# Optimization experiments

Hardware: AMD Instinct MI355X
Metric: run time of the kernel (lower is better)

The kernel has to match this reference:

```python
import jax, jax.numpy as jnp
import numpy as np

NUM_ORI = 20
DEGREE = 2
EPS = 1e-5

def _gelu(x):
    return jax.nn.gelu(x, approximate=False)

def _poly(x, degree=DEGREE):
    # PolynomialFeatures: concat of tensor powers 1..degree+1 of last dim
    feats = [x]
    cur = x
    for _ in range(degree):
        cur = (cur[..., :, None] * x[..., None, :]).reshape(x.shape[:-1] + (-1,))
        feats.append(cur)
    return jnp.concatenate(feats, axis=-1)

def setup_inputs():
    key = jax.random.key(0)
    ks = jax.random.split(key, 16)
    B, N, O, Cin, C, L = 1, 160, NUM_ORI, 16, 128, 2
    basis = C
    def w(k, shape, fan_in):
        return jax.random.normal(k, shape, jnp.float32) / np.sqrt(fan_in).astype(np.float32)
    return {
        "x": jax.random.normal(ks[0], (B, N, O, Cin), jnp.float32),
        "pos": jax.random.normal(ks[1], (B, N, 2), jnp.float32),
        "bw1": w(ks[2], (14, C), 14), "bb1": jnp.zeros((C,), jnp.float32),
        "bw2": w(ks[3], (C, basis), C), "bb2": jnp.zeros((basis,), jnp.float32),
        "fw1": w(ks[4], (3, C), 3), "fb1": jnp.zeros((C,), jnp.float32),
        "fw2": w(ks[5], (C, basis), C), "fb2": jnp.zeros((basis,), jnp.float32),
        "emb_w": w(ks[6], (Cin, C), Cin),
        "kernel_w": w(ks[7], (L, basis, C), basis),
        "fiber_w": w(ks[8], (L, basis, C), basis),
        "conv_b": jnp.zeros((L, C), jnp.float32),
        "ln_g": jnp.ones((L, C), jnp.float32), "ln_b": jnp.zeros((L, C), jnp.float32),
        "mlp_w1": w(ks[9], (L, C, 4 * C), C), "mlp_b1": jnp.zeros((L, 4 * C), jnp.float32),
        "mlp_w2": w(ks[10], (L, 4 * C, C), 4 * C), "mlp_b2": jnp.zeros((L, C), jnp.float32),
    }

def reference(x, pos, bw1, bb1, bw2, bb2, fw1, fb1, fw2, fb2, emb_w,
              kernel_w, fiber_w, conv_b, ln_g, ln_b, mlp_w1, mlp_b1, mlp_w2, mlp_b2):
    # uniform grid of orientations on the circle (GridGenerator(2, num_ori))
    theta = jnp.arange(NUM_ORI, dtype=jnp.float32) * (2.0 * jnp.pi / NUM_ORI)
    ori = jnp.stack([jnp.cos(theta), jnp.sin(theta)], axis=-1)              # [O,2]
    rel = pos[:, None, :, None, :] - pos[:, :, None, None, :]               # [B,M,N,1,2]
    inv1 = jnp.sum(rel * ori[None, None, None], axis=-1, keepdims=True)     # [B,M,N,O,1]
    inv2 = jnp.linalg.norm(rel - rel * inv1, axis=-1, keepdims=True)        # [B,M,N,O,1]
    spat = jnp.concatenate([inv1, inv2], axis=-1)                           # [B,M,N,O,2]
    kb = _gelu(_gelu(_poly(spat) @ bw1 + bb1) @ bw2 + bb2)                  # [B,M,N,O,basis]
    oi = jnp.sum(ori[:, None] * ori[None], axis=-1, keepdims=True)          # [P,O,1]
    fkb = _gelu(_gelu(_poly(oi) @ fw1 + fb1) @ fw2 + fb2)                   # [P,O,basis]
    h = x @ emb_w                                                           # [B,N,O,C]
    C = emb_w.shape[1]
    for l in range(kernel_w.shape[0]):
        kern = kb @ kernel_w[l]                                             # [B,M,N,O,C]
        fk = fkb @ fiber_w[l]                                               # [P,O,C]
        x1 = jnp.einsum('bnoc,bmnoc->bmoc', h, kern)                        # spatial conv
        x2 = jnp.einsum('bmoc,poc->bmpc', x1, fk) / C + conv_b[l]           # fiber conv (depthwise)
        mu = jnp.mean(x2, axis=-1, keepdims=True)
        var = jnp.var(x2, axis=-1, keepdims=True)
        xn = (x2 - mu) / jnp.sqrt(var + EPS) * ln_g[l] + ln_b[l]            # LayerNorm
        mid = _gelu(xn @ mlp_w1[l] + mlp_b1[l])                             # bottleneck MLP
        h = h + (mid @ mlp_w2[l] + mlp_b2[l])                               # residual (layer_scale=None)
    return h
```

## Files before the change

### kernel.cpp

```cpp
#include <hip/hip_runtime.h>
#include <math.h>

#define NORI 20
#define NPTS 160
#define CDIM 128
#define TWO_PI_OVER_O (6.28318530717958647692f / 20.0f)
#define SW 132
#define SAS 136
#define SCL 256.0f
#define ISCL 0.00390625f

typedef __attribute__((ext_vector_type(8))) _Float16 half8v;
typedef __attribute__((ext_vector_type(4))) float float4v;

__device__ __forceinline__ float gelu_exact(float x) {
    float t  = 0.70710678118654752440f * x;
    float at = fabsf(t);
    float tau = __builtin_amdgcn_rcpf(fmaf(0.3275911f, at, 1.0f));
    float p = fmaf(1.061405429f, tau, -1.453152027f);
    p = fmaf(p, tau, 1.421413741f);
    p = fmaf(p, tau, -0.284496736f);
    p = fmaf(p, tau, 0.254829592f);
    p = p * tau;
    float e = __expf(-t * t);
    float erf_abs = fmaf(-p, e, 1.0f);
    float erf_t = copysignf(erf_abs, t);
    return 0.5f * x * (1.0f + erf_t);
}
__device__ __forceinline__ float4 ld4(const float* p) { return *(const float4*)p; }
__device__ __forceinline__ unsigned short f16b(float f) {
    _Float16 h = (_Float16)f;
    return __builtin_bit_cast(unsigned short, h);
}
__device__ __forceinline__ float f16tof(unsigned short u) {
    return (float)__builtin_bit_cast(_Float16, u);
}

#define FMA4(d, s, v) { d.x += (s)*(v).x; d.y += (s)*(v).y; d.z += (s)*(v).z; d.w += (s)*(v).w; }
#define GELU4(d) { d.x = gelu_exact(d.x); d.y = gelu_exact(d.y); \
                   d.z = gelu_exact(d.z); d.w = gelu_exact(d.w); }

__global__ __launch_bounds__(128) void fk_kernel(
    const float* __restrict__ fw1, const float* __restrict__ fb1,
    const float* __restrict__ fw2, const float* __restrict__ fb2,
    const float* __restrict__ fiber_w, unsigned short* __restrict__ fk)
{
    __shared__ float s_u[CDIM];
    __shared__ float s_z[CDIM];
    int bid = blockIdx.x;
    int l = bid / 400;
    int rem = bid % 400;
    int p = rem / 20, o = rem % 20;
    int j = threadIdx.x;

    float t = cosf(TWO_PI_OVER_O * (float)(p - o));
    float f1 = t * t, f2 = f1 * t;

    float u = gelu_exact(t * fw1[j] + f1 * fw1[CDIM + j] + f2 * fw1[2 * CDIM + j] + fb1[j]);
    s_u[j] = u;
    __syncthreads();

    float z0 = 0.f, z1 = 0.f, z2 = 0.f, z3 = 0.f;
    for (int i = 0; i < CDIM; i += 4) {
        z0 += s_u[i    ] * fw2[(i    ) * CDIM + j];
        z1 += s_u[i + 1] * fw2[(i + 1) * CDIM + j];
        z2 += s_u[i + 2] * fw2[(i + 2) * CDIM + j];
        z3 += s_u[i + 3] * fw2[(i + 3) * CDIM + j];
    }
    float z = gelu_exact(((z0 + z1) + (z2 + z3)) + fb2[j]);
    s_z[j] = z;
    __syncthreads();

    const float* fw = fiber_w + l * CDIM * CDIM;
    float a0 = 0.f, a1 = 0.f, a2 = 0.f, a3 = 0.f;
    for (int i = 0; i < CDIM; i += 4) {
        a0 += s_z[i    ] * fw[(i    ) * CDIM + j];
        a1 += s_z[i + 1] * fw[(i + 1) * CDIM + j];
        a2 += s_z[i + 2] * fw[(i + 2) * CDIM + j];
        a3 += s_z[i + 3] * fw[(i + 3) * CDIM + j];
    }
    fk[bid * CDIM + j] = f16b((a0 + a1) + (a2 + a3));
}

__global__ __launch_bounds__(128) void h0_kernel(
    const float* __restrict__ x, const float* __restrict__ emb_w,
    float* __restrict__ h)
{
    int row = blockIdx.x;
    int j = threadIdx.x;
    const float* xr = x + row * 16;
    float acc = 0.f;
#pragma unroll
    for (int i = 0; i < 16; ++i) acc += xr[i] * emb_w[i * CDIM + j];
    h[row * CDIM + j] = acc;
}

__global__ __launch_bounds__(128) void wt_kernel(
    const float* __restrict__ bw2, const float* __restrict__ kernel_w,
    unsigned short* __restrict__ wt)
{
    int b = blockIdx.x;
    int mat = b >> 7, c = b & 127;
    const float* src = (mat == 0) ? bw2 : (kernel_w + (mat - 1) * CDIM * CDIM);
    int k = threadIdx.x;
    wt[(mat * CDIM + c) * CDIM + k] = f16b(src[k * CDIM + c]);
}

#define FOR_BANDS(X) X(0) X(1) X(2) X(3) X(4) X(5) X(6) X(7) X(8) X(9)

#define DECL_ACC(B) float4v acc##B##_0 = {0.f,0.f,0.f,0.f}, acc##B##_1 = {0.f,0.f,0.f,0.f};

#define LDB(PTR, COL, KT) (*(const half8v*)((PTR) + (COL) * CDIM + (KT) * 32 + lh8))

#define LOADB(P, PTR) \
    half8v P##0_0 = LDB(PTR, col0, 0), P##0_1 = LDB(PTR, col1, 0); \
    half8v P##1_0 = LDB(PTR, col0, 1), P##1_1 = LDB(PTR, col1, 1); \
    half8v P##2_0 = LDB(PTR, col0, 2), P##2_1 = LDB(PTR, col1, 2); \
    half8v P##3_0 = LDB(PTR, col0, 3), P##3_1 = LDB(PTR, col1, 3);

#define G_BAND(B, P) { \
    const unsigned short* ar_ = s_act + (B) * 16 * SAS + abase; \
    half8v a0_ = *(const half8v*)(ar_); \
    half8v a1_ = *(const half8v*)(ar_ + 32); \
    half8v a2_ = *(const half8v*)(ar_ + 64); \
    half8v a3_ = *(const half8v*)(ar_ + 96); \
    acc##B##_0 = __builtin_amdgcn_mfma_f32_16x16x32_f16(a0_, P##0_0, acc##B##_0, 0, 0, 0); \
    acc##B##_1 = __builtin_amdgcn_mfma_f32_16x16x32_f16(a0_, P##0_1, acc##B##_1, 0, 0, 0); \
    acc##B##_0 = __builtin_amdgcn_mfma_f32_16x16x32_f16(a1_, P##1_0, acc##B##_0, 0, 0, 0); \
    acc##B##_1 = __builtin_amdgcn_mfma_f32_16x16x32_f16(a1_, P##1_1, acc##B##_1, 0, 0, 0); \
    acc##B##_0 = __builtin_amdgcn_mfma_f32_16x16x32_f16(a2_, P##2_0, acc##B##_0, 0, 0, 0); \
    acc##B##_1 = __builtin_amdgcn_mfma_f32_16x16x32_f16(a2_, P##2_1, acc##B##_1, 0, 0, 0); \
    acc##B##_0 = __builtin_amdgcn_mfma_f32_16x16x32_f16(a3_, P##3_0, acc##B##_0, 0, 0, 0); \
    acc##B##_1 = __builtin_amdgcn_mfma_f32_16x16x32_f16(a3_, P##3_1, acc##B##_1, 0, 0, 0); }

#define G1(B) G_BAND(B, bwf)
#define G2(B) G_BAND(B, kwf)

#define ZW_BAND(B) { \
    int rb_ = (B) * 16 + lh4; \
    s_act[(rb_ + 0) * SAS + col0] = f16b(gelu_exact(fmaf(SCL, acc##B##_0.x, zb0)) * ISCL); \
    s_act[(rb_ + 1) * SAS + col0] = f16b(gelu_exact(fmaf(SCL, acc##B##_0.y, zb0)) * ISCL); \
    s_act[(rb_ + 2) * SAS + col0] = f16b(gelu_exact(fmaf(SCL, acc##B##_0.z, zb0)) * ISCL); \
    s_act[(rb_ + 3) * SAS + col0] = f16b(gelu_exact(fmaf(SCL, acc##B##_0.w, zb0)) * ISCL); \
    s_act[(rb_ + 0) * SAS + col1] = f16b(gelu_exact(fmaf(SCL, acc##B##_1.x, zb1)) * ISCL); \
    s_act[(rb_ + 1) * SAS + col1] = f16b(gelu_exact(fmaf(SCL, acc##B##_1.y, zb1)) * ISCL); \
    s_act[(rb_ + 2) * SAS + col1] = f16b(gelu_exact(fmaf(SCL, acc##B##_1.z, zb1)) * ISCL); \
    s_act[(rb_ + 3) * SAS + col1] = f16b(gelu_exact(fmaf(SCL, acc##B##_1.w, zb1)) * ISCL); \
    acc##B##_0 = vzero; acc##B##_1 = vzero; }

#define H_BAND(B) { \
    int nb_ = (B) * 16 + lh4; \
    xacc0 += acc##B##_0.x * hb0[(nb_ + 0) * 2560]; \
    xacc0 += acc##B##_0.y * hb0[(nb_ + 1) * 2560]; \
    xacc0 += acc##B##_0.z * hb0[(nb_ + 2) * 2560]; \
    xacc0 += acc##B##_0.w * hb0[(nb_ + 3) * 2560]; \
    xacc1 += acc##B##_1.x * hb1[(nb_ + 0) * 2560]; \
    xacc1 += acc##B##_1.y * hb1[(nb_ + 1) * 2560]; \
    xacc1 += acc##B##_1.z * hb1[(nb_ + 2) * 2560]; \
    xacc1 += acc##B##_1.w * hb1[(nb_ + 3) * 2560]; }

__global__ __launch_bounds__(256, 2) void x1_kernel(
    const float* __restrict__ pos, const float* __restrict__ h,
    const float* __restrict__ bw1, const float* __restrict__ bb1,
    const float* __restrict__ bb2,
    const unsigned short* __restrict__ wtb,
    const unsigned short* __restrict__ wtk,
    float* __restrict__ x1)
{
    __shared__ __align__(16) unsigned short s_act[160 * SAS];
    __shared__ float s_bw1[9 * SW];
    __shared__ float s_bb1[CDIM];

    const int tid = threadIdx.x;
    const int rg = tid & 15;
    const int cgv = tid >> 4;
    const int c0u = cgv << 3;

    if (tid < CDIM) {
        const int c = tid;
        s_bw1[0 * SW + c] = bw1[0 * CDIM + c];
        s_bw1[1 * SW + c] = bw1[1 * CDIM + c];
        s_bw1[2 * SW + c] = bw1[2 * CDIM + c];
        s_bw1[3 * SW + c] = bw1[3 * CDIM + c] + bw1[4 * CDIM + c];
        s_bw1[4 * SW + c] = bw1[5 * CDIM + c];
        s_bw1[5 * SW + c] = bw1[6 * CDIM + c];
        s_bw1[6 * SW + c] = bw1[7 * CDIM + c] + bw1[8 * CDIM + c] + bw1[10 * CDIM + c];
        s_bw1[7 * SW + c] = bw1[9 * CDIM + c] + bw1[11 * CDIM + c] + bw1[12 * CDIM + c];
        s_bw1[8 * SW + c] = bw1[13 * CDIM + c];
        s_bb1[c] = bb1[c];
    }

    const int m = blockIdx.x / NORI;
    const int o = blockIdx.x % NORI;
    const float th = TWO_PI_OVER_O * (float)o;
    const float ox = cosf(th), oy = sinf(th);
    const float pmx = pos[2 * m], pmy = pos[2 * m + 1];

    __syncthreads();

#pragma unroll
    for (int rr = 0; rr < 10; ++rr) {
        const int row = rr * 16 + rg;
        float rx = pos[2 * row] - pmx, ry = pos[2 * row + 1] - pmy;
        float ia = rx * ox + ry * oy;
        float ib = sqrtf(rx * rx + ry * ry) * fabsf(1.0f - ia);
        float q2a = ia * ia, q2m = ia * ib, q2b = ib * ib;
        float q3a = q2a * ia, q3m = q2a * ib, q3n = q2m * ib, q3b = q2b * ib;
        float4 ua = ld4(&s_bb1[c0u]);
        float4 ub = ld4(&s_bb1[c0u + 4]);
#define UF(I, S) { float4 wa_ = ld4(&s_bw1[(I) * SW + c0u]); \
                   float4 wb_ = ld4(&s_bw1[(I) * SW + c0u + 4]); \
                   FMA4(ua, S, wa_); FMA4(ub, S, wb_); }
        UF(0, ia) UF(1, ib) UF(2, q2a) UF(3, q2m) UF(4, q2b)
        UF(5, q3a) UF(6, q3m) UF(7, q3n) UF(8, q3b)
#undef UF
        GELU4(ua) GELU4(ub)
        uint4 up;
        up.x = (unsigned int)f16b(ua.x * ISCL) | ((unsigned int)f16b(ua.y * ISCL) << 16);
        up.y = (unsigned int)f16b(ua.z * ISCL) | ((unsigned int)f16b(ua.w * ISCL) << 16);
        up.z = (unsigned int)f16b(ub.x * ISCL) | ((unsigned int)f16b(ub.y * ISCL) << 16);
        up.w = (unsigned int)f16b(ub.z * ISCL) | ((unsigned int)f16b(ub.w * ISCL) << 16);
        *(uint4*)&s_act[row * SAS + c0u] = up;
    }

    const int lane = tid & 63;
    const int wv = tid >> 6;
    const int li = lane & 15;
    const int lh = lane >> 4;
    const int lh8 = lh << 3, lh4 = lh << 2;
    const int col0 = wv * 32 + li;
    const int col1 = col0 + 16;
    const int abase = li * SAS + lh8;
    const float4v vzero = {0.f, 0.f, 0.f, 0.f};

    FOR_BANDS(DECL_ACC)
    LOADB(bwf, wtb)
    __syncthreads();

    FOR_BANDS(G1)
    __syncthreads();

    const float zb0 = bb2[col0], zb1 = bb2[col1];
    FOR_BANDS(ZW_BAND)
    LOADB(kwf, wtk)
    __syncthreads();

    FOR_BANDS(G2)

    const float* hb0 = h + o * CDIM + col0;
    const float* hb1 = h + o * CDIM + col1;
    float xacc0 = 0.f, xacc1 = 0.f;
    FOR_BANDS(H_BAND)

    xacc0 += __shfl_xor(xacc0, 16, 64);
    xacc0 += __shfl_xor(xacc0, 32, 64);
    xacc1 += __shfl_xor(xacc1, 16, 64);
    xacc1 += __shfl_xor(xacc1, 32, 64);

    if (lane < 16) {
        float* x1p = x1 + (m * NORI + o) * CDIM;
        x1p[col0] = xacc0 * SCL;
        x1p[col1] = xacc1 * SCL;
    }
}

__global__ __launch_bounds__(128) void mlp_kernel(
    const float* __restrict__ x1, const unsigned short* __restrict__ fk_l,
    const float* __restrict__ conv_b, const float* __restrict__ ln_g,
    const float* __restrict__ ln_b,
    const float* __restrict__ w1, const float* __restrict__ b1,
    const float* __restrict__ w2, const float* __restrict__ b2,
    float* __restrict__ h)
{
    __shared__ float s_xn[4][132];
    __shared__ float s_mid[4][520];
    __shared__ float s_s1[4][2], s_sq[4][2];

    const int c = threadIdx.x;
    const int m = blockIdx.x / 5, pg = blockIdx.x % 5;
    const int lane = c & 63, wid = c >> 6;

    float x1v[NORI];
#pragma unroll
    for (int o = 0; o < NORI; ++o) x1v[o] = x1[(m * NORI + o) * CDIM + c];

    float x2v[4];
#pragma unroll
    for (int rr = 0; rr < 4; ++rr) {
        int p = pg * 4 + rr;
        float x2 = 0.f;
#pragma unroll
        for (int o = 0; o < NORI; ++o) x2 += x1v[o] * f16tof(fk_l[(p * NORI + o) * CDIM + c]);
        x2 = x2 * (1.0f / 128.0f) + conv_b[c];
        x2v[rr] = x2;
        float s1 = x2, sq = x2 * x2;
        for (int off = 32; off; off >>= 1) {
            s1 += __shfl_down(s1, off, 64);
            sq += __shfl_down(sq, off, 64);
        }
        if (lane == 0) { s_s1[rr][wid] = s1; s_sq[rr][wid] = sq; }
    }
    __syncthreads();
#pragma unroll
    for (int rr = 0; rr < 4; ++rr) {
        float mu  = (s_s1[rr][0] + s_s1[rr][1]) * (1.0f / 128.0f);
        float var = (s_sq[rr][0] + s_sq[rr][1]) * (1.0f / 128.0f) - mu * mu;
        float xn = (x2v[rr] - mu) * rsqrtf(var + 1e-5f) * ln_g[c] + ln_b[c];
        s_xn[rr][c] = xn;
    }
    __syncthreads();

#pragma unroll
    for (int kq = 0; kq < 4; ++kq) {
        int k = kq * CDIM + c;
        float b = b1[k];
        float ac0 = b, ac1 = b, ac2 = b, ac3 = b;
        for (int i = 0; i < CDIM; ++i) {
            float w = w1[i * 512 + k];
            ac0 += s_xn[0][i] * w;
            ac1 += s_xn[1][i] * w;
            ac2 += s_xn[2][i] * w;
            ac3 += s_xn[3][i] * w;
        }
        s_mid[0][k] = gelu_exact(ac0);
        s_mid[1][k] = gelu_exact(ac1);
        s_mid[2][k] = gelu_exact(ac2);
        s_mid[3][k] = gelu_exact(ac3);
    }
    __syncthreads();

    float ao0 = 0.f, ao1 = 0.f, ao2 = 0.f, ao3 = 0.f;
    for (int k = 0; k < 512; ++k) {
        float w = w2[k * CDIM + c];
        ao0 += s_mid[0][k] * w;
        ao1 += s_mid[1][k] * w;
        ao2 += s_mid[2][k] * w;
        ao3 += s_mid[3][k] * w;
    }
    float bb = b2[c];
    h[(m * NORI + pg * 4 + 0) * CDIM + c] += ao0 + bb;
    h[(m * NORI + pg * 4 + 1) * CDIM + c] += ao1 + bb;
    h[(m * NORI + pg * 4 + 2) * CDIM + c] += ao2 + bb;
    h[(m * NORI + pg * 4 + 3) * CDIM + c] += ao3 + bb;
}

extern "C" void kernel_launch(void* const* d_in, const int* in_sizes, int n_in,
                              void* d_out, int out_size, void* d_ws, size_t ws_size,
                              hipStream_t stream)
{
    const float* x        = (const float*)d_in[0];
    const float* pos      = (const float*)d_in[1];
    const float* bw1      = (const float*)d_in[2];
    const float* bb1      = (const float*)d_in[3];
    const float* bw2      = (const float*)d_in[4];
    const float* bb2      = (const float*)d_in[5];
    const float* fw1      = (const float*)d_in[6];
    const float* fb1      = (const float*)d_in[7];
    const float* fw2      = (const float*)d_in[8];
    const float* fb2      = (const float*)d_in[9];
    const float* emb_w    = (const float*)d_in[10];
    const float* kernel_w = (const float*)d_in[11];
    const float* fiber_w  = (const float*)d_in[12];
    const float* conv_b   = (const float*)d_in[13];
    const float* ln_g     = (const float*)d_in[14];
    const float* ln_b     = (const float*)d_in[15];
    const float* mlp_w1   = (const float*)d_in[16];
    const float* mlp_b1   = (const float*)d_in[17];
    const float* mlp_w2   = (const float*)d_in[18];
    const float* mlp_b2   = (const float*)d_in[19];

    float* h = (float*)d_out;

    unsigned short* wt = (unsigned short*)d_ws;
    unsigned short* fk = wt + 3 * CDIM * CDIM;
    float* x1 = (float*)(fk + 2 * NORI * NORI * CDIM);

    wt_kernel<<<3 * CDIM, 128, 0, stream>>>(bw2, kernel_w, wt);
    fk_kernel<<<2 * NORI * NORI, 128, 0, stream>>>(fw1, fb1, fw2, fb2, fiber_w, fk);
    h0_kernel<<<NPTS * NORI, 128, 0, stream>>>(x, emb_w, h);

    for (int l = 0; l < 2; ++l) {
        x1_kernel<<<NPTS * NORI, 256, 0, stream>>>(
            pos, h, bw1, bb1, bb2, wt, wt + (1 + l) * CDIM * CDIM, x1);
        mlp_kernel<<<NPTS * NORI / 4, 128, 0, stream>>>(
            x1, fk + l * NORI * NORI * CDIM,
            conv_b + l * CDIM, ln_g + l * CDIM, ln_b + l * CDIM,
            mlp_w1 + l * CDIM * 4 * CDIM, mlp_b1 + l * 4 * CDIM,
            mlp_w2 + l * 4 * CDIM * CDIM, mlp_b2 + l * CDIM, h);
    }
}
```

Baseline: 318.1 us.

## Split x1 kernel across eight waves with one MFMA column tile each

The x1 kernel moves from 256 to 512 threads per block. Each wave now owns a single 16-column output tile instead of two, which halves the accumulator registers per lane and the per-thread work in the basis-feature stage. The launch bound is raised to allow more resident waves to hide latency. Smaller tweaks rewrite GELU as a single fma on |x/2| and pack f16 pairs with cvt_pkrtz, which changes rounding to round-toward-zero. The trade-off is more threads contending for the same LDS and syncthreads per block.

```diff
diff --git a/kernel.cpp b/kernel.cpp
--- a/kernel.cpp
+++ b/kernel.cpp
@@ -24,8 +24,8 @@
     p = p * tau;
     float e = __expf(-t * t);
     float erf_abs = fmaf(-p, e, 1.0f);
-    float erf_t = copysignf(erf_abs, t);
-    return 0.5f * x * (1.0f + erf_t);
+    float hx = 0.5f * x;
+    return fmaf(fabsf(hx), erf_abs, hx);
 }
 __device__ __forceinline__ float4 ld4(const float* p) { return *(const float4*)p; }
 __device__ __forceinline__ unsigned short f16b(float f) {
@@ -34,6 +34,10 @@
 }
 __device__ __forceinline__ float f16tof(unsigned short u) {
     return (float)__builtin_bit_cast(_Float16, u);
+}
+__device__ __forceinline__ unsigned int pkrtz(float a, float b) {
+    auto h = __builtin_amdgcn_cvt_pkrtz(a, b);
+    return __builtin_bit_cast(unsigned int, h);
 }
 
 #define FMA4(d, s, v) { d.x += (s)*(v).x; d.y += (s)*(v).y; d.z += (s)*(v).z; d.w += (s)*(v).w; }
@@ -108,15 +112,15 @@
 
 #define FOR_BANDS(X) X(0) X(1) X(2) X(3) X(4) X(5) X(6) X(7) X(8) X(9)
 
-#define DECL_ACC(B) float4v acc##B##_0 = {0.f,0.f,0.f,0.f}, acc##B##_1 = {0.f,0.f,0.f,0.f};
-
-#define LDB(PTR, COL, KT) (*(const half8v*)((PTR) + (COL) * CDIM + (KT) * 32 + lh8))
+#define DECL_ACC(B) float4v acc##B = {0.f,0.f,0.f,0.f};
+
+#define LDB(PTR, KT) (*(const half8v*)((PTR) + col0 * CDIM + (KT) * 32 + lh8))
 
 #define LOADB(P, PTR) \
-    half8v P##0_0 = LDB(PTR, col0, 0), P##0_1 = LDB(PTR, col1, 0); \
-    half8v P##1_0 = LDB(PTR, col0, 1), P##1_1 = LDB(PTR, col1, 1); \
-    half8v P##2_0 = LDB(PTR, col0, 2), P##2_1 = LDB(PTR, col1, 2); \
-    half8v P##3_0 = LDB(PTR, col0, 3), P##3_1 = LDB(PTR, col1, 3);
+    half8v P##0 = LDB(PTR, 0); \
+    half8v P##1 = LDB(PTR, 1); \
+    half8v P##2 = LDB(PTR, 2); \
+    half8v P##3 = LDB(PTR, 3);
 
 #define G_BAND(B, P) { \
     const unsigned short* ar_ = s_act + (B) * 16 * SAS + abase; \
@@ -124,42 +128,30 @@
     half8v a1_ = *(const half8v*)(ar_ + 32); \
     half8v a2_ = *(const half8v*)(ar_ + 64); \
     half8v a3_ = *(const half8v*)(ar_ + 96); \
-    acc##B##_0 = __builtin_amdgcn_mfma_f32_16x16x32_f16(a0_, P##0_0, acc##B##_0, 0, 0, 0); \
-    acc##B##_1 = __builtin_amdgcn_mfma_f32_16x16x32_f16(a0_, P##0_1, acc##B##_1, 0, 0, 0); \
-    acc##B##_0 = __builtin_amdgcn_mfma_f32_16x16x32_f16(a1_, P##1_0, acc##B##_0, 0, 0, 0); \
-    acc##B##_1 = __builtin_amdgcn_mfma_f32_16x16x32_f16(a1_, P##1_1, acc##B##_1, 0, 0, 0); \
-    acc##B##_0 = __builtin_amdgcn_mfma_f32_16x16x32_f16(a2_, P##2_0, acc##B##_0, 0, 0, 0); \
-    acc##B##_1 = __builtin_amdgcn_mfma_f32_16x16x32_f16(a2_, P##2_1, acc##B##_1, 0, 0, 0); \
-    acc##B##_0 = __builtin_amdgcn_mfma_f32_16x16x32_f16(a3_, P##3_0, acc##B##_0, 0, 0, 0); \
-    acc##B##_1 = __builtin_amdgcn_mfma_f32_16x16x32_f16(a3_, P##3_1, acc##B##_1, 0, 0, 0); }
+    acc##B = __builtin_amdgcn_mfma_f32_16x16x32_f16(a0_, P##0, acc##B, 0, 0, 0); \
+    acc##B = __builtin_amdgcn_mfma_f32_16x16x32_f16(a1_, P##1, acc##B, 0, 0, 0); \
+    acc##B = __builtin_amdgcn_mfma_f32_16x16x32_f16(a2_, P##2, acc##B, 0, 0, 0); \
+    acc##B = __builtin_amdgcn_mfma_f32_16x16x32_f16(a3_, P##3, acc##B, 0, 0, 0); }
 
 #define G1(B) G_BAND(B, bwf)
 #define G2(B) G_BAND(B, kwf)
 
 #define ZW_BAND(B) { \
     int rb_ = (B) * 16 + lh4; \
-    s_act[(rb_ + 0) * SAS + col0] = f16b(gelu_exact(fmaf(SCL, acc##B##_0.x, zb0)) * ISCL); \
-    s_act[(rb_ + 1) * SAS + col0] = f16b(gelu_exact(fmaf(SCL, acc##B##_0.y, zb0)) * ISCL); \
-    s_act[(rb_ + 2) * SAS + col0] = f16b(gelu_exact(fmaf(SCL, acc##B##_0.z, zb0)) * ISCL); \
-    s_act[(rb_ + 3) * SAS + col0] = f16b(gelu_exact(fmaf(SCL, acc##B##_0.w, zb0)) * ISCL); \
-    s_act[(rb_ + 0) * SAS + col1] = f16b(gelu_exact(fmaf(SCL, acc##B##_1.x, zb1)) * ISCL); \
-    s_act[(rb_ + 1) * SAS + col1] = f16b(gelu_exact(fmaf(SCL, acc##B##_1.y, zb1)) * ISCL); \
-    s_act[(rb_ + 2) * SAS + col1] = f16b(gelu_exact(fmaf(SCL, acc##B##_1.z, zb1)) * ISCL); \
-    s_act[(rb_ + 3) * SAS + col1] = f16b(gelu_exact(fmaf(SCL, acc##B##_1.w, zb1)) * ISCL); \
-    acc##B##_0 = vzero; acc##B##_1 = vzero; }
+    s_act[(rb_ + 0) * SAS + col0] = f16b(gelu_exact(fmaf(SCL, acc##B.x, zb0)) * ISCL); \
+    s_act[(rb_ + 1) * SAS + col0] = f16b(gelu_exact(fmaf(SCL, acc##B.y, zb0)) * ISCL); \
+    s_act[(rb_ + 2) * SAS + col0] = f16b(gelu_exact(fmaf(SCL, acc##B.z, zb0)) * ISCL); \
+    s_act[(rb_ + 3) * SAS + col0] = f16b(gelu_exact(fmaf(SCL, acc##B.w, zb0)) * ISCL); \
+    acc##B = vzero; }
 
 #define H_BAND(B) { \
     int nb_ = (B) * 16 + lh4; \
-    xacc0 += acc##B##_0.x * hb0[(nb_ + 0) * 2560]; \
-    xacc0 += acc##B##_0.y * hb0[(nb_ + 1) * 2560]; \
-    xacc0 += acc##B##_0.z * hb0[(nb_ + 2) * 2560]; \
-    xacc0 += acc##B##_0.w * hb0[(nb_ + 3) * 2560]; \
-    xacc1 += acc##B##_1.x * hb1[(nb_ + 0) * 2560]; \
-    xacc1 += acc##B##_1.y * hb1[(nb_ + 1) * 2560]; \
-    xacc1 += acc##B##_1.z * hb1[(nb_ + 2) * 2560]; \
-    xacc1 += acc##B##_1.w * hb1[(nb_ + 3) * 2560]; }
-
-__global__ __launch_bounds__(256, 2) void x1_kernel(
+    xacc0 += acc##B.x * hb0[(nb_ + 0) * 2560]; \
+    xacc0 += acc##B.y * hb0[(nb_ + 1) * 2560]; \
+    xacc0 += acc##B.z * hb0[(nb_ + 2) * 2560]; \
+    xacc0 += acc##B.w * hb0[(nb_ + 3) * 2560]; }
+
+__global__ __launch_bounds__(512, 6) void x1_kernel(
     const float* __restrict__ pos, const float* __restrict__ h,
     const float* __restrict__ bw1, const float* __restrict__ bb1,
     const float* __restrict__ bb2,
@@ -172,8 +164,8 @@
     __shared__ float s_bb1[CDIM];
 
     const int tid = threadIdx.x;
-    const int rg = tid & 15;
-    const int cgv = tid >> 4;
+    const int rg = tid & 31;
+    const int cgv = tid >> 5;
     const int c0u = cgv << 3;
 
     if (tid < CDIM) {
@@ -199,8 +191,8 @@
     __syncthreads();
 
 #pragma unroll
-    for (int rr = 0; rr < 10; ++rr) {
-        const int row = rr * 16 + rg;
+    for (int rr = 0; rr < 5; ++rr) {
+        const int row = rr * 32 + rg;
         float rx = pos[2 * row] - pmx, ry = pos[2 * row + 1] - pmy;
         float ia = rx * ox + ry * oy;
         float ib = sqrtf(rx * rx + ry * ry) * fabsf(1.0f - ia);
@@ -216,10 +208,10 @@
 #undef UF
         GELU4(ua) GELU4(ub)
         uint4 up;
-        up.x = (unsigned int)f16b(ua.x * ISCL) | ((unsigned int)f16b(ua.y * ISCL) << 16);
-        up.y = (unsigned int)f16b(ua.z * ISCL) | ((unsigned int)f16b(ua.w * ISCL) << 16);
-        up.z = (unsigned int)f16b(ub.x * ISCL) | ((unsigned int)f16b(ub.y * ISCL) << 16);
-        up.w = (unsigned int)f16b(ub.z * ISCL) | ((unsigned int)f16b(ub.w * ISCL) << 16);
+        up.x = pkrtz(ua.x * ISCL, ua.y * ISCL);
+        up.y = pkrtz(ua.z * ISCL, ua.w * ISCL);
+        up.z = pkrtz(ub.x * ISCL, ub.y * ISCL);
+        up.w = pkrtz(ub.z * ISCL, ub.w * ISCL);
         *(uint4*)&s_act[row * SAS + c0u] = up;
     }
 
@@ -228,8 +220,7 @@
     const int li = lane & 15;
     const int lh = lane >> 4;
     const int lh8 = lh << 3, lh4 = lh << 2;
-    const int col0 = wv * 32 + li;
-    const int col1 = col0 + 16;
+    const int col0 = wv * 16 + li;
     const int abase = li * SAS + lh8;
     const float4v vzero = {0.f, 0.f, 0.f, 0.f};
 
@@ -240,7 +231,7 @@
     FOR_BANDS(G1)
     __syncthreads();
 
-    const float zb0 = bb2[col0], zb1 = bb2[col1];
+    const float zb0 = bb2[col0];
     FOR_BANDS(ZW_BAND)
     LOADB(kwf, wtk)
     __syncthreads();
@@ -248,20 +239,14 @@
     FOR_BANDS(G2)
 
     const float* hb0 = h + o * CDIM + col0;
-    const float* hb1 = h + o * CDIM + col1;
-    float xacc0 = 0.f, xacc1 = 0.f;
+    float xacc0 = 0.f;
     FOR_BANDS(H_BAND)
 
     xacc0 += __shfl_xor(xacc0, 16, 64);
     xacc0 += __shfl_xor(xacc0, 32, 64);
-    xacc1 += __shfl_xor(xacc1, 16, 64);
-    xacc1 += __shfl_xor(xacc1, 32, 64);
-
-    if (lane < 16) {
-        float* x1p = x1 + (m * NORI + o) * CDIM;
-        x1p[col0] = xacc0 * SCL;
-        x1p[col1] = xacc1 * SCL;
-    }
+
+    if (lane < 16)
+        x1[(m * NORI + o) * CDIM + col0] = xacc0 * SCL;
 }
 
 __global__ __launch_bounds__(128) void mlp_kernel(
@@ -380,7 +365,7 @@
     h0_kernel<<<NPTS * NORI, 128, 0, stream>>>(x, emb_w, h);
 
     for (int l = 0; l < 2; ++l) {
-        x1_kernel<<<NPTS * NORI, 256, 0, stream>>>(
+        x1_kernel<<<NPTS * NORI, 512, 0, stream>>>(
             pos, h, bw1, bb1, bb2, wt, wt + (1 + l) * CDIM * CDIM, x1);
         mlp_kernel<<<NPTS * NORI / 4, 128, 0, stream>>>(
             x1, fk + l * NORI * NORI * CDIM,
```

Result: slower. 591.1 us (+85.8%).
